# Kernel optimization log

Measured on AMD Instinct MI355X. Metric: run time of the kernel, lower is better.

The kernel has to match this reference:

```python
import jax, jax.numpy as jnp
import numpy as np

B, IN_DIM, D, C = 8192, 2048, 1024, 1000


def setup_inputs() -> dict:
    key = jax.random.key(0)
    k1, k2, k3 = jax.random.split(key, 3)
    x = jax.random.normal(k1, (B, IN_DIM), dtype=jnp.float32)
    W_enc = jax.random.normal(k2, (IN_DIM, D), dtype=jnp.float32) * 0.02
    b_enc = jnp.zeros((D,), dtype=jnp.float32)
    prototypes = jax.random.normal(k3, (C, D), dtype=jnp.float32)
    return {"x": x, "W_enc": W_enc, "b_enc": b_enc, "prototypes": prototypes}


def reference(x, W_enc, b_enc, prototypes):
    # Encoder features Z: [B, D] (stand-in for model.forward_encoder)
    Z = x @ W_enc + b_enc
    # MSELoss(Z[i], proto[j]) = mean over D of squared diff
    # = (||z||^2 + ||p||^2 - 2 z.p) / D  -- avoids [B, C, D] intermediate
    z2 = jnp.sum(Z * Z, axis=-1, keepdims=True)          # [B, 1]
    p2 = jnp.sum(prototypes * prototypes, axis=-1)[None]  # [1, C]
    cross = jnp.einsum("bd,cd->bc", Z, prototypes)        # [B, C]
    mse = (z2 + p2 - 2.0 * cross) / jnp.asarray(Z.shape[-1], Z.dtype)
    return -mse
```

## Files before the change

kernel.cpp:

```cpp
#include <hip/hip_runtime.h>

#define B_ROWS 8192
#define IN_DIM 2048
#define D_DIM  1024
#define C_CLS  1000

typedef __attribute__((ext_vector_type(8))) short   bf16x8;
typedef __attribute__((ext_vector_type(4))) float   f32x4;

__device__ __forceinline__ float b2f(unsigned short s) {
    unsigned int u = ((unsigned int)s) << 16;
    return __builtin_bit_cast(float, u);
}
__device__ __forceinline__ unsigned short f2b(float f) {
    unsigned int u = __builtin_bit_cast(unsigned int, f);
    u = u + 0x7fffu + ((u >> 16) & 1u);
    return (unsigned short)(u >> 16);
}

__device__ __forceinline__ void g2lds16(const void* g, void* l) {
    __builtin_amdgcn_global_load_lds(
        (const __attribute__((address_space(1))) unsigned int*)g,
        (__attribute__((address_space(3))) unsigned int*)l,
        16, 0, 0);
}

__global__ __launch_bounds__(256) void k_xb(const float* __restrict__ x,
                                            unsigned short* __restrict__ xb) {
    const size_t i = ((size_t)blockIdx.x * 256 + threadIdx.x) * 8;
    float4 v0 = *(const float4*)(x + i);
    float4 v1 = *(const float4*)(x + i + 4);
    bf16x8 h;
    h[0] = (short)f2b(v0.x); h[1] = (short)f2b(v0.y);
    h[2] = (short)f2b(v0.z); h[3] = (short)f2b(v0.w);
    h[4] = (short)f2b(v1.x); h[5] = (short)f2b(v1.y);
    h[6] = (short)f2b(v1.z); h[7] = (short)f2b(v1.w);
    *(bf16x8*)(xb + i) = h;
}

__global__ __launch_bounds__(256) void k_wt(const float* __restrict__ W,
                                            unsigned short* __restrict__ Wt) {
    __shared__ float t[32][33];
    const int tid = threadIdx.x;
    const int tx = tid & 31, ty = tid >> 5;
    const int kb = (blockIdx.x & 63) * 32;
    const int nb = (blockIdx.x >> 6) * 32;
#pragma unroll
    for (int j = 0; j < 4; ++j)
        t[ty + 8 * j][tx] = W[(size_t)(kb + ty + 8 * j) * D_DIM + nb + tx];
    __syncthreads();
#pragma unroll
    for (int j = 0; j < 4; ++j)
        Wt[(size_t)(nb + ty + 8 * j) * IN_DIM + kb + tx] = f2b(t[tx][ty + 8 * j]);
}

__global__ __launch_bounds__(256) void k_proto(const float* __restrict__ P,
                                               unsigned short* __restrict__ Pb,
                                               float* __restrict__ p2) {
    const int c = blockIdx.x;
    const int tid = threadIdx.x;
    float s = 0.f;
    if (c < C_CLS) {
        float4 v = *((const float4*)(P + (size_t)c * D_DIM) + tid);
        s = v.x * v.x + v.y * v.y + v.z * v.z + v.w * v.w;
        ushort4 h; h.x = f2b(v.x); h.y = f2b(v.y); h.z = f2b(v.z); h.w = f2b(v.w);
        *((ushort4*)(Pb + (size_t)c * D_DIM) + tid) = h;
    } else {
        ushort4 h; h.x = 0; h.y = 0; h.z = 0; h.w = 0;
        *((ushort4*)(Pb + (size_t)c * D_DIM) + tid) = h;
    }
#pragma unroll
    for (int o = 32; o > 0; o >>= 1) s += __shfl_down(s, o);
    __shared__ float red[4];
    if ((tid & 63) == 0) red[tid >> 6] = s;
    __syncthreads();
    if (tid == 0) p2[c] = red[0] + red[1] + red[2] + red[3];
}

__global__ __launch_bounds__(256) void k_z2r(const float* __restrict__ z2p,
                                             float* __restrict__ z2) {
    const int r = blockIdx.x * 256 + threadIdx.x;
    float s = 0.f;
#pragma unroll
    for (int j = 0; j < 16; ++j) s += z2p[j * B_ROWS + r];
    z2[r] = s;
}

template <int MODE>
__global__ __launch_bounds__(512, 2) void k_gemm8(
    const unsigned short* __restrict__ Ab,
    const unsigned short* __restrict__ Bt,
    const float* __restrict__ bias,
    const float* __restrict__ z2,
    const float* __restrict__ p2,
    unsigned short* __restrict__ Zout,
    float* __restrict__ z2p,
    float* __restrict__ Out) {
    constexpr int K  = (MODE == 0) ? IN_DIM : D_DIM;
    constexpr int NT = K / 64;
    constexpr unsigned ASZ = 256 * 64 * 2;
    constexpr unsigned BSZ = 128 * 64 * 2;
    extern __shared__ char lds[];
    char* pa0 = lds;            char* pa1 = lds + ASZ;  char* pa2 = lds + 2 * ASZ;
    char* pb0 = lds + 3 * ASZ;  char* pb1 = pb0 + BSZ;  char* pb2 = pb0 + 2 * BSZ;

    const int tid  = threadIdx.x;
    const int wave = tid >> 6, lane = tid & 63;
    const int lo = lane & 15, hi = lane >> 4;
    const int wm = wave >> 1, wn = wave & 1;

    const int swz = ((blockIdx.x & 7) << 5) + (blockIdx.x >> 3);
    const int bm = swz >> 3, bn = swz & 7;
    const int rowbase = bm * 256, colbase = bn * 128;

    const int srow   = lane >> 3;
    const int gchunk = (lane & 7) ^ (srow & 7);

    auto STAGE_A = [&](char* dst, int kt, int i) {
        const int s = i * 8 + wave;
        g2lds16(Ab + (size_t)(rowbase + s * 8 + srow) * K + kt * 64 + gchunk * 8,
                dst + s * 1024);
    };
    auto STAGE_B = [&](char* dst, int kt, int i) {
        const int s = i * 8 + wave;
        g2lds16(Bt + (size_t)(colbase + s * 8 + srow) * K + kt * 64 + gchunk * 8,
                dst + s * 1024);
    };

    f32x4 acc[4][4];
#pragma unroll
    for (int m = 0; m < 4; ++m)
#pragma unroll
        for (int n = 0; n < 4; ++n) acc[m][n] = (f32x4){0.f, 0.f, 0.f, 0.f};

#pragma unroll
    for (int i = 0; i < 4; ++i) STAGE_A(pa0, 0, i);
#pragma unroll
    for (int i = 0; i < 2; ++i) STAGE_B(pb0, 0, i);
#pragma unroll
    for (int i = 0; i < 4; ++i) STAGE_A(pa1, 1, i);
#pragma unroll
    for (int i = 0; i < 2; ++i) STAGE_B(pb1, 1, i);
    asm volatile("s_waitcnt vmcnt(6)" ::: "memory");
    __builtin_amdgcn_s_barrier();

    auto PHASE = [&](int ks, int stg, int kt2) {
        bf16x8 af[4], bfr[4];
#pragma unroll
        for (int m = 0; m < 4; ++m) {
            const int row = wm * 64 + m * 16 + lo;
            unsigned addr = (unsigned)(row * 128 + ks * 64 + hi * 16)
                          ^ (unsigned)((lo & 7) << 4);
            af[m] = *(const bf16x8*)(pa0 + addr);
        }
#pragma unroll
        for (int n = 0; n < 4; ++n) {
            const int row = wn * 64 + n * 16 + lo;
            unsigned addr = (unsigned)(row * 128 + ks * 64 + hi * 16)
                          ^ (unsigned)((lo & 7) << 4);
            bfr[n] = *(const bf16x8*)(pb0 + addr);
        }
        if (stg == 1) { STAGE_A(pa2, kt2, 0); STAGE_A(pa2, kt2, 1); STAGE_B(pb2, kt2, 0); }
        if (stg == 2) { STAGE_A(pa2, kt2, 2); STAGE_A(pa2, kt2, 3); STAGE_B(pb2, kt2, 1); }
        __builtin_amdgcn_s_barrier();
        __builtin_amdgcn_s_setprio(1);
#pragma unroll
        for (int m = 0; m < 4; ++m)
#pragma unroll
            for (int n = 0; n < 4; ++n)
                acc[m][n] = __builtin_amdgcn_mfma_f32_16x16x32_bf16(
                    af[m], bfr[n], acc[m][n], 0, 0, 0);
        __builtin_amdgcn_s_setprio(0);
    };
    auto ROTATE = [&]() {
        char* t;
        t = pa0; pa0 = pa1; pa1 = pa2; pa2 = t;
        t = pb0; pb0 = pb1; pb1 = pb2; pb2 = t;
    };

    for (int t = 0; t < NT - 2; ++t) {
        PHASE(0, 1, t + 2);
        __builtin_amdgcn_s_barrier();
        PHASE(1, 2, t + 2);
        asm volatile("s_waitcnt vmcnt(6)" ::: "memory");
        __builtin_amdgcn_s_barrier();
        ROTATE();
    }
    PHASE(0, 0, 0);
    __builtin_amdgcn_s_barrier();
    PHASE(1, 0, 0);
    asm volatile("s_waitcnt vmcnt(0)" ::: "memory");
    __builtin_amdgcn_s_barrier();
    ROTATE();
    PHASE(0, 0, 0);
    __builtin_amdgcn_s_barrier();
    PHASE(1, 0, 0);

    if constexpr (MODE == 0) {
        float bv[4];
#pragma unroll
        for (int n = 0; n < 4; ++n) bv[n] = bias[colbase + wn * 64 + n * 16 + lo];
#pragma unroll
        for (int m = 0; m < 4; ++m)
#pragma unroll
            for (int r = 0; r < 4; ++r) {
                const int rg = rowbase + wm * 64 + m * 16 + hi * 4 + r;
                float s = 0.f;
#pragma unroll
                for (int n = 0; n < 4; ++n) {
                    const float zf = acc[m][n][r] + bv[n];
                    Zout[(size_t)rg * D_DIM + colbase + wn * 64 + n * 16 + lo] = f2b(zf);
                    s += zf * zf;
                }
                s += __shfl_xor(s, 1); s += __shfl_xor(s, 2);
                s += __shfl_xor(s, 4); s += __shfl_xor(s, 8);
                if (lo == 0) z2p[(size_t)(bn * 2 + wn) * B_ROWS + rg] = s;
            }
    } else {
        float p2v[4];
#pragma unroll
        for (int n = 0; n < 4; ++n) p2v[n] = p2[colbase + wn * 64 + n * 16 + lo];
#pragma unroll
        for (int m = 0; m < 4; ++m)
#pragma unroll
            for (int r = 0; r < 4; ++r) {
                const int rg = rowbase + wm * 64 + m * 16 + hi * 4 + r;
                const float zv = z2[rg];
#pragma unroll
                for (int n = 0; n < 4; ++n) {
                    const int cg = colbase + wn * 64 + n * 16 + lo;
                    if (cg < C_CLS)
                        Out[(size_t)rg * C_CLS + cg] =
                            (2.f * acc[m][n][r] - zv - p2v[n]) * (1.f / 1024.f);
                }
            }
    }
}

extern "C" void kernel_launch(void* const* d_in, const int* in_sizes, int n_in,
                              void* d_out, int out_size, void* d_ws, size_t ws_size,
                              hipStream_t stream) {
    const float* x = (const float*)d_in[0];
    const float* W = (const float*)d_in[1];
    const float* b = (const float*)d_in[2];
    const float* P = (const float*)d_in[3];
    float* out = (float*)d_out;

    char* ws = (char*)d_ws;
    unsigned short* Wt  = (unsigned short*)(ws);
    unsigned short* Pb  = (unsigned short*)(ws + (4  << 20));
    unsigned short* Zb  = (unsigned short*)(ws + (6  << 20));
    float*          z2  = (float*)(ws + (22 << 20));
    float*          p2  = (float*)(ws + (22 << 20) + (64 << 10));
    float*          z2p = (float*)(ws + (22 << 20) + (128 << 10));
    unsigned short* xb  = (unsigned short*)(ws + (23 << 20));

    const unsigned lds_bytes = 3 * (256 * 64 * 2) + 3 * (128 * 64 * 2);

    k_wt<<<dim3(2048), dim3(256), 0, stream>>>(W, Wt);
    k_proto<<<dim3(1024), dim3(256), 0, stream>>>(P, Pb, p2);
    k_xb<<<dim3(8192), dim3(256), 0, stream>>>(x, xb);
    k_gemm8<0><<<dim3(256), dim3(512), lds_bytes, stream>>>(
        xb, Wt, b, nullptr, nullptr, Zb, z2p, nullptr);
    k_z2r<<<dim3(32), dim3(256), 0, stream>>>(z2p, z2);
    k_gemm8<1><<<dim3(256), dim3(512), lds_bytes, stream>>>(
        Zb, Pb, nullptr, z2, p2, nullptr, nullptr, out);
}
```

Measured before the change: 88.53 us.

## Fuse x fp32-to-bf16 conversion into GEMM A-load and merge small prep kernels

```diff
diff --git a/kernel.cpp b/kernel.cpp
--- a/kernel.cpp
+++ b/kernel.cpp
@@ -8,16 +8,16 @@
 typedef __attribute__((ext_vector_type(8))) short   bf16x8;
 typedef __attribute__((ext_vector_type(4))) float   f32x4;
 
-__device__ __forceinline__ float b2f(unsigned short s) {
-    unsigned int u = ((unsigned int)s) << 16;
-    return __builtin_bit_cast(float, u);
-}
 __device__ __forceinline__ unsigned short f2b(float f) {
     unsigned int u = __builtin_bit_cast(unsigned int, f);
     u = u + 0x7fffu + ((u >> 16) & 1u);
     return (unsigned short)(u >> 16);
 }
-
+__device__ __forceinline__ unsigned cvtpk(float lo, float hi) {
+    unsigned r;
+    asm("v_cvt_pk_bf16_f32 %0, %1, %2" : "=v"(r) : "v"(lo), "v"(hi));
+    return r;
+}
 __device__ __forceinline__ void g2lds16(const void* g, void* l) {
     __builtin_amdgcn_global_load_lds(
         (const __attribute__((address_space(1))) unsigned int*)g,
@@ -25,76 +25,55 @@
         16, 0, 0);
 }
 
-__global__ __launch_bounds__(256) void k_xb(const float* __restrict__ x,
-                                            unsigned short* __restrict__ xb) {
-    const size_t i = ((size_t)blockIdx.x * 256 + threadIdx.x) * 8;
-    float4 v0 = *(const float4*)(x + i);
-    float4 v1 = *(const float4*)(x + i + 4);
-    bf16x8 h;
-    h[0] = (short)f2b(v0.x); h[1] = (short)f2b(v0.y);
-    h[2] = (short)f2b(v0.z); h[3] = (short)f2b(v0.w);
-    h[4] = (short)f2b(v1.x); h[5] = (short)f2b(v1.y);
-    h[6] = (short)f2b(v1.z); h[7] = (short)f2b(v1.w);
-    *(bf16x8*)(xb + i) = h;
-}
-
-__global__ __launch_bounds__(256) void k_wt(const float* __restrict__ W,
-                                            unsigned short* __restrict__ Wt) {
-    __shared__ float t[32][33];
+__global__ __launch_bounds__(256) void k_pre(const float* __restrict__ W,
+                                             const float* __restrict__ P,
+                                             unsigned short* __restrict__ Wt,
+                                             unsigned short* __restrict__ Pb,
+                                             float* __restrict__ p2) {
     const int tid = threadIdx.x;
-    const int tx = tid & 31, ty = tid >> 5;
-    const int kb = (blockIdx.x & 63) * 32;
-    const int nb = (blockIdx.x >> 6) * 32;
-#pragma unroll
-    for (int j = 0; j < 4; ++j)
-        t[ty + 8 * j][tx] = W[(size_t)(kb + ty + 8 * j) * D_DIM + nb + tx];
-    __syncthreads();
-#pragma unroll
-    for (int j = 0; j < 4; ++j)
-        Wt[(size_t)(nb + ty + 8 * j) * IN_DIM + kb + tx] = f2b(t[tx][ty + 8 * j]);
-}
-
-__global__ __launch_bounds__(256) void k_proto(const float* __restrict__ P,
-                                               unsigned short* __restrict__ Pb,
-                                               float* __restrict__ p2) {
-    const int c = blockIdx.x;
-    const int tid = threadIdx.x;
-    float s = 0.f;
-    if (c < C_CLS) {
-        float4 v = *((const float4*)(P + (size_t)c * D_DIM) + tid);
-        s = v.x * v.x + v.y * v.y + v.z * v.z + v.w * v.w;
-        ushort4 h; h.x = f2b(v.x); h.y = f2b(v.y); h.z = f2b(v.z); h.w = f2b(v.w);
-        *((ushort4*)(Pb + (size_t)c * D_DIM) + tid) = h;
+    if (blockIdx.x < 2048) {
+        __shared__ float t[32][33];
+        const int tx = tid & 31, ty = tid >> 5;
+        const int kb = (blockIdx.x & 63) * 32;
+        const int nb = (blockIdx.x >> 6) * 32;
+#pragma unroll
+        for (int j = 0; j < 4; ++j)
+            t[ty + 8 * j][tx] = W[(size_t)(kb + ty + 8 * j) * D_DIM + nb + tx];
+        __syncthreads();
+#pragma unroll
+        for (int j = 0; j < 4; ++j)
+            Wt[(size_t)(nb + ty + 8 * j) * IN_DIM + kb + tx] = f2b(t[tx][ty + 8 * j]);
     } else {
-        ushort4 h; h.x = 0; h.y = 0; h.z = 0; h.w = 0;
-        *((ushort4*)(Pb + (size_t)c * D_DIM) + tid) = h;
-    }
-#pragma unroll
-    for (int o = 32; o > 0; o >>= 1) s += __shfl_down(s, o);
-    __shared__ float red[4];
-    if ((tid & 63) == 0) red[tid >> 6] = s;
-    __syncthreads();
-    if (tid == 0) p2[c] = red[0] + red[1] + red[2] + red[3];
-}
-
-__global__ __launch_bounds__(256) void k_z2r(const float* __restrict__ z2p,
-                                             float* __restrict__ z2) {
-    const int r = blockIdx.x * 256 + threadIdx.x;
-    float s = 0.f;
-#pragma unroll
-    for (int j = 0; j < 16; ++j) s += z2p[j * B_ROWS + r];
-    z2[r] = s;
+        const int c = blockIdx.x - 2048;
+        float s = 0.f;
+        if (c < C_CLS) {
+            float4 v = *((const float4*)(P + (size_t)c * D_DIM) + tid);
+            s = v.x * v.x + v.y * v.y + v.z * v.z + v.w * v.w;
+            ushort4 h; h.x = f2b(v.x); h.y = f2b(v.y); h.z = f2b(v.z); h.w = f2b(v.w);
+            *((ushort4*)(Pb + (size_t)c * D_DIM) + tid) = h;
+        } else {
+            ushort4 h; h.x = 0; h.y = 0; h.z = 0; h.w = 0;
+            *((ushort4*)(Pb + (size_t)c * D_DIM) + tid) = h;
+        }
+#pragma unroll
+        for (int o = 32; o > 0; o >>= 1) s += __shfl_down(s, o);
+        __shared__ float red[4];
+        if ((tid & 63) == 0) red[tid >> 6] = s;
+        __syncthreads();
+        if (tid == 0) p2[c] = red[0] + red[1] + red[2] + red[3];
+    }
 }
 
 template <int MODE>
 __global__ __launch_bounds__(512, 2) void k_gemm8(
+    const float* __restrict__ Axf,
     const unsigned short* __restrict__ Ab,
     const unsigned short* __restrict__ Bt,
     const float* __restrict__ bias,
-    const float* __restrict__ z2,
+    const float* __restrict__ z2p_in,
     const float* __restrict__ p2,
     unsigned short* __restrict__ Zout,
-    float* __restrict__ z2p,
+    float* __restrict__ z2p_out,
     float* __restrict__ Out) {
     constexpr int K  = (MODE == 0) ? IN_DIM : D_DIM;
     constexpr int NT = K / 64;
@@ -103,6 +82,7 @@
     extern __shared__ char lds[];
     char* pa0 = lds;            char* pa1 = lds + ASZ;  char* pa2 = lds + 2 * ASZ;
     char* pb0 = lds + 3 * ASZ;  char* pb1 = pb0 + BSZ;  char* pb2 = pb0 + 2 * BSZ;
+    float* z2loc = (float*)(lds + 3 * (ASZ + BSZ));
 
     const int tid  = threadIdx.x;
     const int wave = tid >> 6, lane = tid & 63;
@@ -116,16 +96,38 @@
     const int srow   = lane >> 3;
     const int gchunk = (lane & 7) ^ (srow & 7);
 
-    auto STAGE_A = [&](char* dst, int kt, int i) {
-        const int s = i * 8 + wave;
-        g2lds16(Ab + (size_t)(rowbase + s * 8 + srow) * K + kt * 64 + gchunk * 8,
-                dst + s * 1024);
-    };
     auto STAGE_B = [&](char* dst, int kt, int i) {
         const int s = i * 8 + wave;
         g2lds16(Bt + (size_t)(colbase + s * 8 + srow) * K + kt * 64 + gchunk * 8,
                 dst + s * 1024);
     };
+    auto STAGE_A_ASY = [&](char* dst, int kt, int i) {
+        const int s = i * 8 + wave;
+        g2lds16(Ab + (size_t)(rowbase + s * 8 + srow) * K + kt * 64 + gchunk * 8,
+                dst + s * 1024);
+    };
+
+    const int arow  = tid >> 1;
+    const int ahalf = tid & 1;
+    float4 areg[8];
+    auto LOADA = [&](int kt) {
+        const float4* gp =
+            (const float4*)(Axf + (size_t)(rowbase + arow) * K + kt * 64 + ahalf * 32);
+#pragma unroll
+        for (int i = 0; i < 8; ++i) areg[i] = gp[i];
+    };
+    auto WRITEA = [&](char* dst) {
+#pragma unroll
+        for (int j = 0; j < 4; ++j) {
+            uint4 w;
+            w.x = cvtpk(areg[2 * j].x,     areg[2 * j].y);
+            w.y = cvtpk(areg[2 * j].z,     areg[2 * j].w);
+            w.z = cvtpk(areg[2 * j + 1].x, areg[2 * j + 1].y);
+            w.w = cvtpk(areg[2 * j + 1].z, areg[2 * j + 1].w);
+            const int c = ahalf * 4 + j;
+            *(uint4*)(dst + arow * 128 + ((c ^ (arow & 7)) << 4)) = w;
+        }
+    };
 
     f32x4 acc[4][4];
 #pragma unroll
@@ -133,44 +135,58 @@
 #pragma unroll
         for (int n = 0; n < 4; ++n) acc[m][n] = (f32x4){0.f, 0.f, 0.f, 0.f};
 
-#pragma unroll
-    for (int i = 0; i < 4; ++i) STAGE_A(pa0, 0, i);
-#pragma unroll
-    for (int i = 0; i < 2; ++i) STAGE_B(pb0, 0, i);
-#pragma unroll
-    for (int i = 0; i < 4; ++i) STAGE_A(pa1, 1, i);
-#pragma unroll
-    for (int i = 0; i < 2; ++i) STAGE_B(pb1, 1, i);
-    asm volatile("s_waitcnt vmcnt(6)" ::: "memory");
+    if constexpr (MODE == 0) {
+        LOADA(0);
+        STAGE_B(pb0, 0, 0); STAGE_B(pb0, 0, 1);
+        WRITEA(pa0);
+        LOADA(1);
+        STAGE_B(pb1, 1, 0); STAGE_B(pb1, 1, 1);
+        WRITEA(pa1);
+        asm volatile("s_waitcnt lgkmcnt(0)" ::: "memory");
+    } else {
+        if (tid < 256) {
+            float s = 0.f;
+#pragma unroll
+            for (int j = 0; j < 16; ++j) s += z2p_in[j * B_ROWS + rowbase + tid];
+            z2loc[tid] = s;
+        }
+#pragma unroll
+        for (int i = 0; i < 4; ++i) STAGE_A_ASY(pa0, 0, i);
+        STAGE_B(pb0, 0, 0); STAGE_B(pb0, 0, 1);
+#pragma unroll
+        for (int i = 0; i < 4; ++i) STAGE_A_ASY(pa1, 1, i);
+        STAGE_B(pb1, 1, 0); STAGE_B(pb1, 1, 1);
+        asm volatile("s_waitcnt vmcnt(6) lgkmcnt(0)" ::: "memory");
+    }
     __builtin_amdgcn_s_barrier();
 
-    auto PHASE = [&](int ks, int stg, int kt2) {
-        bf16x8 af[4], bfr[4];
-#pragma unroll
-        for (int m = 0; m < 4; ++m) {
-            const int row = wm * 64 + m * 16 + lo;
-            unsigned addr = (unsigned)(row * 128 + ks * 64 + hi * 16)
-                          ^ (unsigned)((lo & 7) << 4);
-            af[m] = *(const bf16x8*)(pa0 + addr);
-        }
-#pragma unroll
-        for (int n = 0; n < 4; ++n) {
-            const int row = wn * 64 + n * 16 + lo;
-            unsigned addr = (unsigned)(row * 128 + ks * 64 + hi * 16)
-                          ^ (unsigned)((lo & 7) << 4);
-            bfr[n] = *(const bf16x8*)(pb0 + addr);
-        }
-        if (stg == 1) { STAGE_A(pa2, kt2, 0); STAGE_A(pa2, kt2, 1); STAGE_B(pb2, kt2, 0); }
-        if (stg == 2) { STAGE_A(pa2, kt2, 2); STAGE_A(pa2, kt2, 3); STAGE_B(pb2, kt2, 1); }
-        __builtin_amdgcn_s_barrier();
-        __builtin_amdgcn_s_setprio(1);
-#pragma unroll
-        for (int m = 0; m < 4; ++m)
-#pragma unroll
-            for (int n = 0; n < 4; ++n)
-                acc[m][n] = __builtin_amdgcn_mfma_f32_16x16x32_bf16(
-                    af[m], bfr[n], acc[m][n], 0, 0, 0);
-        __builtin_amdgcn_s_setprio(0);
+    auto COMPUTE = [&]() {
+#pragma unroll
+        for (int ks = 0; ks < 2; ++ks) {
+            bf16x8 af[4], bfr[4];
+#pragma unroll
+            for (int m = 0; m < 4; ++m) {
+                const int row = wm * 64 + m * 16 + lo;
+                unsigned addr = (unsigned)(row * 128 + ks * 64 + hi * 16)
+                              ^ (unsigned)((lo & 7) << 4);
+                af[m] = *(const bf16x8*)(pa0 + addr);
+            }
+#pragma unroll
+            for (int n = 0; n < 4; ++n) {
+                const int row = wn * 64 + n * 16 + lo;
+                unsigned addr = (unsigned)(row * 128 + ks * 64 + hi * 16)
+                              ^ (unsigned)((lo & 7) << 4);
+                bfr[n] = *(const bf16x8*)(pb0 + addr);
+            }
+            __builtin_amdgcn_s_setprio(1);
+#pragma unroll
+            for (int m = 0; m < 4; ++m)
+#pragma unroll
+                for (int n = 0; n < 4; ++n)
+                    acc[m][n] = __builtin_amdgcn_mfma_f32_16x16x32_bf16(
+                        af[m], bfr[n], acc[m][n], 0, 0, 0);
+            __builtin_amdgcn_s_setprio(0);
+        }
     };
     auto ROTATE = [&]() {
         char* t;
@@ -178,23 +194,32 @@
         t = pb0; pb0 = pb1; pb1 = pb2; pb2 = t;
     };
 
-    for (int t = 0; t < NT - 2; ++t) {
-        PHASE(0, 1, t + 2);
-        __builtin_amdgcn_s_barrier();
-        PHASE(1, 2, t + 2);
-        asm volatile("s_waitcnt vmcnt(6)" ::: "memory");
-        __builtin_amdgcn_s_barrier();
-        ROTATE();
-    }
-    PHASE(0, 0, 0);
-    __builtin_amdgcn_s_barrier();
-    PHASE(1, 0, 0);
-    asm volatile("s_waitcnt vmcnt(0)" ::: "memory");
-    __builtin_amdgcn_s_barrier();
-    ROTATE();
-    PHASE(0, 0, 0);
-    __builtin_amdgcn_s_barrier();
-    PHASE(1, 0, 0);
+    for (int t = 0; t < NT; ++t) {
+        const bool stg = (t < NT - 2);
+        if (stg) {
+            if constexpr (MODE == 0) {
+                LOADA(t + 2);
+                STAGE_B(pb2, t + 2, 0); STAGE_B(pb2, t + 2, 1);
+            } else {
+#pragma unroll
+                for (int i = 0; i < 4; ++i) STAGE_A_ASY(pa2, t + 2, i);
+                STAGE_B(pb2, t + 2, 0); STAGE_B(pb2, t + 2, 1);
+            }
+        }
+        COMPUTE();
+        if (t < NT - 1) {
+            if constexpr (MODE == 0) {
+                if (stg) WRITEA(pa2);
+                if (stg) asm volatile("s_waitcnt vmcnt(2) lgkmcnt(0)" ::: "memory");
+                else     asm volatile("s_waitcnt vmcnt(0) lgkmcnt(0)" ::: "memory");
+            } else {
+                if (stg) asm volatile("s_waitcnt vmcnt(6)" ::: "memory");
+                else     asm volatile("s_waitcnt vmcnt(0)" ::: "memory");
+            }
+            __builtin_amdgcn_s_barrier();
+            ROTATE();
+        }
+    }
 
     if constexpr (MODE == 0) {
         float bv[4];
@@ -214,7 +239,7 @@
                 }
                 s += __shfl_xor(s, 1); s += __shfl_xor(s, 2);
                 s += __shfl_xor(s, 4); s += __shfl_xor(s, 8);
-                if (lo == 0) z2p[(size_t)(bn * 2 + wn) * B_ROWS + rg] = s;
+                if (lo == 0) z2p_out[(size_t)(bn * 2 + wn) * B_ROWS + rg] = s;
             }
     } else {
         float p2v[4];
@@ -224,8 +249,9 @@
         for (int m = 0; m < 4; ++m)
 #pragma unroll
             for (int r = 0; r < 4; ++r) {
-                const int rg = rowbase + wm * 64 + m * 16 + hi * 4 + r;
-                const float zv = z2[rg];
+                const int rl = wm * 64 + m * 16 + hi * 4 + r;
+                const int rg = rowbase + rl;
+                const float zv = z2loc[rl];
 #pragma unroll
                 for (int n = 0; n < 4; ++n) {
                     const int cg = colbase + wn * 64 + n * 16 + lo;
@@ -250,19 +276,14 @@
     unsigned short* Wt  = (unsigned short*)(ws);
     unsigned short* Pb  = (unsigned short*)(ws + (4  << 20));
     unsigned short* Zb  = (unsigned short*)(ws + (6  << 20));
-    float*          z2  = (float*)(ws + (22 << 20));
     float*          p2  = (float*)(ws + (22 << 20) + (64 << 10));
     float*          z2p = (float*)(ws + (22 << 20) + (128 << 10));
-    unsigned short* xb  = (unsigned short*)(ws + (23 << 20));
-
-    const unsigned lds_bytes = 3 * (256 * 64 * 2) + 3 * (128 * 64 * 2);
-
-    k_wt<<<dim3(2048), dim3(256), 0, stream>>>(W, Wt);
-    k_proto<<<dim3(1024), dim3(256), 0, stream>>>(P, Pb, p2);
-    k_xb<<<dim3(8192), dim3(256), 0, stream>>>(x, xb);
+
+    const unsigned lds_bytes = 3 * (256 * 64 * 2 + 128 * 64 * 2) + 1024;
+
+    k_pre<<<dim3(3072), dim3(256), 0, stream>>>(W, P, Wt, Pb, p2);
     k_gemm8<0><<<dim3(256), dim3(512), lds_bytes, stream>>>(
-        xb, Wt, b, nullptr, nullptr, Zb, z2p, nullptr);
-    k_z2r<<<dim3(32), dim3(256), 0, stream>>>(z2p, z2);
+        x, nullptr, Wt, b, nullptr, nullptr, Zb, z2p, nullptr);
     k_gemm8<1><<<dim3(256), dim3(512), lds_bytes, stream>>>(
-        Zb, Pb, nullptr, z2, p2, nullptr, nullptr, out);
-}
+        nullptr, Zb, Pb, nullptr, z2p, p2, nullptr, nullptr, out);
+}
```

New measurement: 130.0 us. 46.8% more time.
